# Kernel tuning notes

Hardware: AMD Instinct MI355X
Metric: run time of the kernel (lower is better)

## Reference

```python
import jax, jax.numpy as jnp
import numpy as np

PC_MIN = jnp.array([-51.2, -51.2, -5.0], dtype=jnp.float32)
PC_MAX = jnp.array([51.2, 51.2, 3.0], dtype=jnp.float32)
H0, W0 = 900, 1600  # original image size used for grid normalization
EPS = 1e-5


def grid_sample_2d(feats, gx, gy):
    # feats: (N,C,H,W); gx,gy: (N,Q) normalized [-1,1]; bilinear, align_corners=False, zero padding
    N, C, H, W = feats.shape
    x = ((gx + 1.0) * W - 1.0) / 2.0
    y = ((gy + 1.0) * H - 1.0) / 2.0
    x0 = jnp.floor(x)
    y0 = jnp.floor(y)
    ff = feats.reshape(N, C, H * W)
    out = jnp.zeros((N, C, gx.shape[1]), dtype=feats.dtype)
    for dx in (0, 1):
        for dy in (0, 1):
            xi = x0 + dx
            yi = y0 + dy
            w = (1.0 - jnp.abs(x - xi)) * (1.0 - jnp.abs(y - yi))
            inb = (xi >= 0) & (xi < W) & (yi >= 0) & (yi < H)
            idx = (jnp.clip(yi, 0, H - 1) * W + jnp.clip(xi, 0, W - 1)).astype(jnp.int32)
            g = jnp.take_along_axis(ff, idx[:, None, :], axis=2)  # (N,C,Q)
            out = out + g * (w * inb)[:, None, :]
    return out


def grid_sample_3d(feats, gx, gy, gz):
    # feats: (B,C,Z,Y,X); gx->X, gy->Y, gz->Z; trilinear, align_corners=False, zero padding
    B, C, Z, Y, X = feats.shape
    x = ((gx + 1.0) * X - 1.0) / 2.0
    y = ((gy + 1.0) * Y - 1.0) / 2.0
    z = ((gz + 1.0) * Z - 1.0) / 2.0
    x0 = jnp.floor(x)
    y0 = jnp.floor(y)
    z0 = jnp.floor(z)
    ff = feats.reshape(B, C, Z * Y * X)
    out = jnp.zeros((B, C, gx.shape[1]), dtype=feats.dtype)
    for dx in (0, 1):
        for dy in (0, 1):
            for dz in (0, 1):
                xi = x0 + dx
                yi = y0 + dy
                zi = z0 + dz
                w = (1.0 - jnp.abs(x - xi)) * (1.0 - jnp.abs(y - yi)) * (1.0 - jnp.abs(z - zi))
                inb = (xi >= 0) & (xi < X) & (yi >= 0) & (yi < Y) & (zi >= 0) & (zi < Z)
                idx = ((jnp.clip(zi, 0, Z - 1) * Y + jnp.clip(yi, 0, Y - 1)) * X + jnp.clip(xi, 0, X - 1)).astype(jnp.int32)
                g = jnp.take_along_axis(ff, idx[:, None, :], axis=2)  # (B,C,Q)
                out = out + g * (w * inb)[:, None, :]
    return out


def layer_norm(x, g, b):
    mu = x.mean(-1, keepdims=True)
    var = ((x - mu) ** 2).mean(-1, keepdims=True)
    return (x - mu) * jax.lax.rsqrt(var + 1e-5) * g + b


def setup_inputs() -> dict:
    key = jax.random.key(0)
    ks = jax.random.split(key, 20)
    B, Q, C, N = 2, 900, 256, 6
    H, W = 112, 200
    Z, Y, X = 10, 128, 128
    s = 0.02
    return {
        'query': jax.random.normal(ks[0], (B, Q, C), jnp.float32),
        'reference_points': jax.random.uniform(ks[1], (B, Q, 3), jnp.float32),
        'img_feats': jax.random.normal(ks[2], (B, N, C, H, W), jnp.float32),
        'lidar_feats': jax.random.normal(ks[3], (B, C, Z, Y, X), jnp.float32),
        'lidar2img': jax.random.normal(ks[4], (B, N, 4, 4), jnp.float32),
        'cam_w': jax.random.normal(ks[5], (C, C), jnp.float32) * s,
        'cam_b': jnp.zeros((C,), jnp.float32),
        'lidar_w': jax.random.normal(ks[6], (C, C), jnp.float32) * s,
        'lidar_b': jnp.zeros((C,), jnp.float32),
        'att_w1': jax.random.normal(ks[7], (C, C // 4), jnp.float32) * s,
        'att_b1': jnp.zeros((C // 4,), jnp.float32),
        'att_w2': jax.random.normal(ks[8], (C // 4, 2), jnp.float32) * s,
        'att_b2': jnp.zeros((2,), jnp.float32),
        'fus_w1': jax.random.normal(ks[9], (2 * C, C), jnp.float32) * s,
        'fus_b1': jnp.zeros((C,), jnp.float32),
        'ln_g': jnp.ones((C,), jnp.float32),
        'ln_b': jnp.zeros((C,), jnp.float32),
        'fus_w2': jax.random.normal(ks[10], (C, C), jnp.float32) * s,
        'fus_b2': jnp.zeros((C,), jnp.float32),
    }


def reference(query, reference_points, img_feats, lidar_feats, lidar2img,
              cam_w, cam_b, lidar_w, lidar_b, att_w1, att_b1, att_w2, att_b2,
              fus_w1, fus_b1, ln_g, ln_b, fus_w2, fus_b2):
    B, Q, _ = query.shape
    N, C = img_feats.shape[1], img_feats.shape[2]
    # ---- camera branch: 3D -> 2D projection + bilinear sample + masked mean over cams ----
    abs_pts = reference_points * (PC_MAX - PC_MIN) + PC_MIN
    homo = jnp.concatenate([abs_pts, jnp.ones_like(abs_pts[..., :1])], -1)  # (B,Q,4)
    cam = jnp.einsum('bnij,bqj->bnqi', lidar2img, homo)  # (B,N,Q,4)
    depth = cam[..., 2]
    dmask = depth > EPS
    dclamp = jnp.maximum(depth, EPS)
    u_n = 2.0 * (cam[..., 0] / dclamp) / (W0 - 1) - 1.0
    v_n = 2.0 * (cam[..., 1] / dclamp) / (H0 - 1) - 1.0
    valid = (u_n >= -1) & (u_n <= 1) & (v_n >= -1) & (v_n <= 1) & dmask  # (B,N,Q)
    Hf, Wf = img_feats.shape[-2], img_feats.shape[-1]
    samp = grid_sample_2d(img_feats.reshape(B * N, C, Hf, Wf),
                          u_n.reshape(B * N, Q), v_n.reshape(B * N, Q))  # (B*N,C,Q)
    samp = samp.reshape(B, N, C, Q).transpose(0, 3, 1, 2)  # (B,Q,N,C)
    vm = valid.transpose(0, 2, 1)[..., None].astype(samp.dtype)  # (B,Q,N,1)
    feat_cam = (samp * vm).sum(2) / jnp.maximum(vm.sum(2), 1.0)  # (B,Q,C)
    # ---- LiDAR branch: 3D trilinear sample ----
    g = reference_points * 2.0 - 1.0
    feat_lid = grid_sample_3d(lidar_feats, g[..., 0], g[..., 1], g[..., 2]).transpose(0, 2, 1)  # (B,Q,C)
    # ---- projections + adaptive gated fusion ----
    feat_cam = feat_cam @ cam_w + cam_b
    feat_lid = feat_lid @ lidar_w + lidar_b
    h = jax.nn.relu(query @ att_w1 + att_b1)
    w = jax.nn.softmax(h @ att_w2 + att_b2, axis=-1)  # (B,Q,2)
    fused = jnp.concatenate([w[..., 0:1] * feat_cam, w[..., 1:2] * feat_lid], -1)
    h2 = jax.nn.relu(layer_norm(fused @ fus_w1 + fus_b1, ln_g, ln_b))  # dropout is identity in eval
    return h2 @ fus_w2 + fus_b2
```

## Files before the change

kernel.cpp:

```cpp
#include <hip/hip_runtime.h>

#define QN 900
#define CN 256
#define NCAM 6
#define HF 112
#define WF 200
#define ZL 10
#define YL 128
#define XL 128
#define R 2

__global__ __launch_bounds__(256) void mafs_fused(
    const float* __restrict__ query,
    const float* __restrict__ rp,
    const float* __restrict__ imgf,
    const float* __restrict__ lidf,
    const float* __restrict__ l2i,
    const float* __restrict__ cam_w, const float* __restrict__ cam_b,
    const float* __restrict__ lid_w, const float* __restrict__ lid_b,
    const float* __restrict__ att_w1, const float* __restrict__ att_b1,
    const float* __restrict__ att_w2, const float* __restrict__ att_b2,
    const float* __restrict__ fus_w1, const float* __restrict__ fus_b1,
    const float* __restrict__ ln_g, const float* __restrict__ ln_b,
    const float* __restrict__ fus_w2, const float* __restrict__ fus_b2,
    float* __restrict__ out)
{
  const int blk = blockIdx.x;
  const int q0  = blk * R;
  const int b   = q0 / QN;
  const int tid = threadIdx.x;
  const int lane = tid & 63, wv = tid >> 6;

  __shared__ float s_q[R*CN];
  __shared__ float s_a[CN*R], s_b[CN*R], s_t[CN*R];
  __shared__ float s_hp[4*64];
  __shared__ float s_w0[R], s_w1[R];
  __shared__ float s_red[16];

  #pragma unroll
  for (int r = 0; r < R; ++r)
    s_q[r*CN + tid] = query[(size_t)(q0+r)*CN + tid];
  __syncthreads();

  {
    const int r  = wv & 1;
    const int kh = wv >> 1;
    const float* qrow = s_q + r*CN + kh*128;
    const float* w1p  = att_w1 + (size_t)kh*128*64;
    float h = 0.f;
    #pragma unroll 4
    for (int k = 0; k < 128; ++k) h += qrow[k] * w1p[k*64 + lane];
    s_hp[wv*64 + lane] = h;
  }
  __syncthreads();
  if (wv < R) {
    const int r = wv;
    float h = s_hp[r*64 + lane] + s_hp[(r+2)*64 + lane] + att_b1[lane];
    h = fmaxf(h, 0.f);
    float l0 = h * att_w2[2*lane], l1 = h * att_w2[2*lane+1];
    #pragma unroll
    for (int o = 32; o > 0; o >>= 1) { l0 += __shfl_down(l0,o); l1 += __shfl_down(l1,o); }
    if (lane == 0) {
      l0 += att_b2[0]; l1 += att_b2[1];
      const float m  = fmaxf(l0, l1);
      const float e0 = expf(l0 - m), e1 = expf(l1 - m);
      const float inv = 1.f / (e0 + e1);
      s_w0[r] = e0 * inv; s_w1[r] = e1 * inv;
    }
  }

  float rxx[R], ryy[R], rzz[R];
  #pragma unroll
  for (int r = 0; r < R; ++r) {
    rxx[r] = rp[(q0+r)*3+0];
    ryy[r] = rp[(q0+r)*3+1];
    rzz[r] = rp[(q0+r)*3+2];
  }

  float lv[R][8], lw[R][8];
  {
    const float* lbase = lidf + ((size_t)(b*CN) + tid) * (ZL*YL*XL);
    #pragma unroll
    for (int r = 0; r < R; ++r) {
      const float x = rxx[r]*(float)XL - 0.5f;
      const float y = ryy[r]*(float)YL - 0.5f;
      const float z = rzz[r]*(float)ZL - 0.5f;
      const float x0f = floorf(x), y0f = floorf(y), z0f = floorf(z);
      const int x0=(int)x0f, y0=(int)y0f, z0=(int)z0f;
      const float fx=x-x0f, fy=y-y0f, fz=z-z0f;
      const float wx[2]={1.f-fx,fx}, wy[2]={1.f-fy,fy}, wz[2]={1.f-fz,fz};
      #pragma unroll
      for (int dz = 0; dz < 2; ++dz)
        #pragma unroll
        for (int dy = 0; dy < 2; ++dy)
          #pragma unroll
          for (int dx = 0; dx < 2; ++dx) {
            const int xi=x0+dx, yi=y0+dy, zi=z0+dz;
            const bool ib = (xi>=0)&&(xi<XL)&&(yi>=0)&&(yi<YL)&&(zi>=0)&&(zi<ZL);
            const int xc=min(max(xi,0),XL-1);
            const int yc=min(max(yi,0),YL-1);
            const int zc=min(max(zi,0),ZL-1);
            const int i=(dz*2+dy)*2+dx;
            lv[r][i] = lbase[(zc*YL+yc)*XL+xc];
            lw[r][i] = ib ? wx[dx]*wy[dy]*wz[dz] : 0.f;
          }
    }
  }

  float fc[R] = {0.f,0.f}, cnt[R] = {0.f,0.f};
  #pragma unroll
  for (int n = 0; n < NCAM; ++n) {
    const float* M = l2i + (size_t)(b*NCAM + n)*16;
    const float m0=M[0],m1=M[1],m2=M[2],m3=M[3];
    const float m4=M[4],m5=M[5],m6=M[6],m7=M[7];
    const float m8=M[8],m9=M[9],m10=M[10],m11=M[11];
    #pragma unroll
    for (int r = 0; r < R; ++r) {
      const float ax = rxx[r]*102.4f - 51.2f;
      const float ay = ryy[r]*102.4f - 51.2f;
      const float az = rzz[r]*8.0f   - 5.0f;
      const float c0 = m0*ax + m1*ay + m2 *az + m3;
      const float c1 = m4*ax + m5*ay + m6 *az + m7;
      const float c2 = m8*ax + m9*ay + m10*az + m11;
      const float dc = fmaxf(c2, 1e-5f);
      const float u = 2.0f * (c0 / dc) / 1599.0f - 1.0f;
      const float v = 2.0f * (c1 / dc) /  899.0f - 1.0f;
      const bool valid = (u >= -1.f) && (u <= 1.f) && (v >= -1.f) && (v <= 1.f)
                         && (c2 > 1e-5f);
      if (valid) {
        cnt[r] += 1.f;
        const float x = ((u + 1.f)*(float)WF - 1.f)*0.5f;
        const float y = ((v + 1.f)*(float)HF - 1.f)*0.5f;
        const float x0f = floorf(x), y0f = floorf(y);
        const int x0=(int)x0f, y0=(int)y0f;
        const float fx=x-x0f, fy=y-y0f;
        const bool xb0=(x0>=0)&&(x0<WF), xb1=(x0+1<WF)&&(x0+1>=0);
        const bool yb0=(y0>=0)&&(y0<HF), yb1=(y0+1<HF)&&(y0+1>=0);
        const float w00 = (xb0&&yb0) ? (1.f-fx)*(1.f-fy) : 0.f;
        const float w10 = (xb1&&yb0) ? fx*(1.f-fy)       : 0.f;
        const float w01 = (xb0&&yb1) ? (1.f-fx)*fy       : 0.f;
        const float w11 = (xb1&&yb1) ? fx*fy             : 0.f;
        const int xc0=min(max(x0,0),WF-1),  xc1=min(max(x0+1,0),WF-1);
        const int yc0=min(max(y0,0),HF-1),  yc1=min(max(y0+1,0),HF-1);
        const float* fb = imgf + ((size_t)((b*NCAM + n)*CN) + tid)*(HF*WF);
        const float t00 = fb[yc0*WF + xc0];
        const float t10 = fb[yc0*WF + xc1];
        const float t01 = fb[yc1*WF + xc0];
        const float t11 = fb[yc1*WF + xc1];
        fc[r] += w00*t00 + w10*t10 + w01*t01 + w11*t11;
      }
    }
  }
  #pragma unroll
  for (int r = 0; r < R; ++r) fc[r] /= fmaxf(cnt[r], 1.f);

  float fl[R];
  #pragma unroll
  for (int r = 0; r < R; ++r) {
    float s = 0.f;
    #pragma unroll
    for (int i = 0; i < 8; ++i) s += lw[r][i] * lv[r][i];
    fl[r] = s;
  }

  #pragma unroll
  for (int r = 0; r < R; ++r) { s_a[tid*R + r] = fc[r]; s_b[tid*R + r] = fl[r]; }
  __syncthreads();

  float pc[R] = {0,0}, pl[R] = {0,0};
  #pragma unroll 4
  for (int k = 0; k < CN; ++k) {
    const float wc = cam_w[k*CN + tid];
    const float wl = lid_w[k*CN + tid];
    const float2 xa = *(const float2*)&s_a[k*R];
    const float2 xb = *(const float2*)&s_b[k*R];
    pc[0] += xa.x*wc; pc[1] += xa.y*wc;
    pl[0] += xb.x*wl; pl[1] += xb.y*wl;
  }
  const float pcb = cam_b[tid], plb = lid_b[tid];
  __syncthreads();
  #pragma unroll
  for (int r = 0; r < R; ++r) {
    s_a[tid*R + r] = s_w0[r] * (pc[r] + pcb);
    s_b[tid*R + r] = s_w1[r] * (pl[r] + plb);
  }
  __syncthreads();

  float t1[R] = {0,0};
  #pragma unroll 2
  for (int k = 0; k < CN; ++k) {
    const float wA = fus_w1[k*CN + tid];
    const float wB = fus_w1[(size_t)(CN + k)*CN + tid];
    const float2 xa = *(const float2*)&s_a[k*R];
    const float2 xb = *(const float2*)&s_b[k*R];
    t1[0] += xa.x*wA + xb.x*wB;
    t1[1] += xa.y*wA + xb.y*wB;
  }
  {
    const float bb = fus_b1[tid];
    t1[0] += bb; t1[1] += bb;
  }

  #pragma unroll
  for (int r = 0; r < R; ++r) {
    float s1 = t1[r];
    #pragma unroll
    for (int o = 32; o > 0; o >>= 1) s1 += __shfl_down(s1, o);
    if (lane == 0) s_red[r*4 + wv] = s1;
  }
  __syncthreads();
  float mu[R];
  #pragma unroll
  for (int r = 0; r < R; ++r)
    mu[r] = (s_red[r*4+0]+s_red[r*4+1]+s_red[r*4+2]+s_red[r*4+3]) * (1.f/256.f);
  #pragma unroll
  for (int r = 0; r < R; ++r) {
    const float d = t1[r] - mu[r];
    float s2 = d*d;
    #pragma unroll
    for (int o = 32; o > 0; o >>= 1) s2 += __shfl_down(s2, o);
    if (lane == 0) s_red[8 + r*4 + wv] = s2;
  }
  __syncthreads();
  {
    const float g = ln_g[tid], be = ln_b[tid];
    #pragma unroll
    for (int r = 0; r < R; ++r) {
      const float var = (s_red[8+r*4+0]+s_red[8+r*4+1]+s_red[8+r*4+2]+s_red[8+r*4+3]) * (1.f/256.f);
      const float ri = rsqrtf(var + 1e-5f);
      s_t[tid*R + r] = fmaxf((t1[r] - mu[r]) * ri * g + be, 0.f);
    }
  }
  __syncthreads();

  float o[R] = {0,0};
  #pragma unroll 4
  for (int k = 0; k < CN; ++k) {
    const float w = fus_w2[k*CN + tid];
    const float2 xt = *(const float2*)&s_t[k*R];
    o[0] += xt.x*w; o[1] += xt.y*w;
  }
  const float ob = fus_b2[tid];
  #pragma unroll
  for (int r = 0; r < R; ++r)
    out[(size_t)(q0+r)*CN + tid] = o[r] + ob;
}

extern "C" void kernel_launch(void* const* d_in, const int* in_sizes, int n_in,
                              void* d_out, int out_size, void* d_ws, size_t ws_size,
                              hipStream_t stream) {
  const float* query   = (const float*)d_in[0];
  const float* rpts    = (const float*)d_in[1];
  const float* imgf    = (const float*)d_in[2];
  const float* lidf    = (const float*)d_in[3];
  const float* l2i     = (const float*)d_in[4];
  const float* cam_w   = (const float*)d_in[5];
  const float* cam_b   = (const float*)d_in[6];
  const float* lid_w   = (const float*)d_in[7];
  const float* lid_b   = (const float*)d_in[8];
  const float* att_w1  = (const float*)d_in[9];
  const float* att_b1  = (const float*)d_in[10];
  const float* att_w2  = (const float*)d_in[11];
  const float* att_b2  = (const float*)d_in[12];
  const float* fus_w1  = (const float*)d_in[13];
  const float* fus_b1  = (const float*)d_in[14];
  const float* ln_g    = (const float*)d_in[15];
  const float* ln_b    = (const float*)d_in[16];
  const float* fus_w2  = (const float*)d_in[17];
  const float* fus_b2  = (const float*)d_in[18];
  float* out = (float*)d_out;

  dim3 grid((2*QN)/R);
  dim3 block(256);
  mafs_fused<<<grid, block, 0, stream>>>(
      query, rpts, imgf, lidf, l2i,
      cam_w, cam_b, lid_w, lid_b,
      att_w1, att_b1, att_w2, att_b2,
      fus_w1, fus_b1, ln_g, ln_b, fus_w2, fus_b2, out);
}
```

Measured before the change: 119.0 us.

## Process four queries per block with 512 threads split into two halves

```diff
diff --git a/kernel.cpp b/kernel.cpp
--- a/kernel.cpp
+++ b/kernel.cpp
@@ -8,9 +8,10 @@
 #define ZL 10
 #define YL 128
 #define XL 128
-#define R 2
-
-__global__ __launch_bounds__(256) void mafs_fused(
+#define R 4
+#define NT 512
+
+__global__ __launch_bounds__(NT, 4) void mafs_fused(
     const float* __restrict__ query,
     const float* __restrict__ rp,
     const float* __restrict__ imgf,
@@ -29,35 +30,36 @@
   const int q0  = blk * R;
   const int b   = q0 / QN;
   const int tid = threadIdx.x;
-  const int lane = tid & 63, wv = tid >> 6;
+  const int c    = tid & 255;
+  const int h    = tid >> 8;
+  const int lane = tid & 63;
+  const int w    = tid >> 6;
 
   __shared__ float s_q[R*CN];
   __shared__ float s_a[CN*R], s_b[CN*R], s_t[CN*R];
-  __shared__ float s_hp[4*64];
+  __shared__ float s_hp[8*64];
   __shared__ float s_w0[R], s_w1[R];
-  __shared__ float s_red[16];
-
-  #pragma unroll
-  for (int r = 0; r < R; ++r)
-    s_q[r*CN + tid] = query[(size_t)(q0+r)*CN + tid];
-  __syncthreads();
-
-  {
-    const int r  = wv & 1;
-    const int kh = wv >> 1;
-    const float* qrow = s_q + r*CN + kh*128;
-    const float* w1p  = att_w1 + (size_t)kh*128*64;
-    float h = 0.f;
+  __shared__ float s_red[2*R*4];
+
+  #pragma unroll
+  for (int i = 0; i < 2; ++i)
+    s_q[i*NT + tid] = query[(size_t)q0*CN + i*NT + tid];
+  __syncthreads();
+
+  {
+    const int rw = w & 3, kh = w >> 2;
+    const float* qrow = s_q + rw*CN + kh*128;
+    const float* w1p  = att_w1 + (size_t)(kh*128)*64;
+    float hh = 0.f;
     #pragma unroll 4
-    for (int k = 0; k < 128; ++k) h += qrow[k] * w1p[k*64 + lane];
-    s_hp[wv*64 + lane] = h;
-  }
-  __syncthreads();
-  if (wv < R) {
-    const int r = wv;
-    float h = s_hp[r*64 + lane] + s_hp[(r+2)*64 + lane] + att_b1[lane];
-    h = fmaxf(h, 0.f);
-    float l0 = h * att_w2[2*lane], l1 = h * att_w2[2*lane+1];
+    for (int k = 0; k < 128; ++k) hh += qrow[k] * w1p[k*64 + lane];
+    s_hp[w*64 + lane] = hh;
+  }
+  __syncthreads();
+  if (w < R) {
+    float hh = s_hp[w*64 + lane] + s_hp[(w+4)*64 + lane] + att_b1[lane];
+    hh = fmaxf(hh, 0.f);
+    float l0 = hh * att_w2[2*lane], l1 = hh * att_w2[2*lane+1];
     #pragma unroll
     for (int o = 32; o > 0; o >>= 1) { l0 += __shfl_down(l0,o); l1 += __shfl_down(l1,o); }
     if (lane == 0) {
@@ -65,26 +67,27 @@
       const float m  = fmaxf(l0, l1);
       const float e0 = expf(l0 - m), e1 = expf(l1 - m);
       const float inv = 1.f / (e0 + e1);
-      s_w0[r] = e0 * inv; s_w1[r] = e1 * inv;
-    }
-  }
-
-  float rxx[R], ryy[R], rzz[R];
-  #pragma unroll
-  for (int r = 0; r < R; ++r) {
-    rxx[r] = rp[(q0+r)*3+0];
-    ryy[r] = rp[(q0+r)*3+1];
-    rzz[r] = rp[(q0+r)*3+2];
-  }
-
-  float lv[R][8], lw[R][8];
-  {
-    const float* lbase = lidf + ((size_t)(b*CN) + tid) * (ZL*YL*XL);
-    #pragma unroll
-    for (int r = 0; r < R; ++r) {
-      const float x = rxx[r]*(float)XL - 0.5f;
-      const float y = ryy[r]*(float)YL - 0.5f;
-      const float z = rzz[r]*(float)ZL - 0.5f;
+      s_w0[w] = e0 * inv; s_w1[w] = e1 * inv;
+    }
+  }
+
+  float rxx[2], ryy[2], rzz[2];
+  #pragma unroll
+  for (int i = 0; i < 2; ++i) {
+    const int r = 2*h + i;
+    rxx[i] = rp[(q0+r)*3+0];
+    ryy[i] = rp[(q0+r)*3+1];
+    rzz[i] = rp[(q0+r)*3+2];
+  }
+
+  float lv[2][8], lw_[2][8];
+  {
+    const float* lbase = lidf + ((size_t)(b*CN) + c) * (ZL*YL*XL);
+    #pragma unroll
+    for (int i = 0; i < 2; ++i) {
+      const float x = rxx[i]*(float)XL - 0.5f;
+      const float y = ryy[i]*(float)YL - 0.5f;
+      const float z = rzz[i]*(float)ZL - 0.5f;
       const float x0f = floorf(x), y0f = floorf(y), z0f = floorf(z);
       const int x0=(int)x0f, y0=(int)y0f, z0=(int)z0f;
       const float fx=x-x0f, fy=y-y0f, fz=z-z0f;
@@ -100,14 +103,14 @@
             const int xc=min(max(xi,0),XL-1);
             const int yc=min(max(yi,0),YL-1);
             const int zc=min(max(zi,0),ZL-1);
-            const int i=(dz*2+dy)*2+dx;
-            lv[r][i] = lbase[(zc*YL+yc)*XL+xc];
-            lw[r][i] = ib ? wx[dx]*wy[dy]*wz[dz] : 0.f;
+            const int t=(dz*2+dy)*2+dx;
+            lv[i][t]  = lbase[(zc*YL+yc)*XL+xc];
+            lw_[i][t] = ib ? wx[dx]*wy[dy]*wz[dz] : 0.f;
           }
     }
   }
 
-  float fc[R] = {0.f,0.f}, cnt[R] = {0.f,0.f};
+  float fc[2] = {0.f,0.f}, cnt[2] = {0.f,0.f};
   #pragma unroll
   for (int n = 0; n < NCAM; ++n) {
     const float* M = l2i + (size_t)(b*NCAM + n)*16;
@@ -115,10 +118,10 @@
     const float m4=M[4],m5=M[5],m6=M[6],m7=M[7];
     const float m8=M[8],m9=M[9],m10=M[10],m11=M[11];
     #pragma unroll
-    for (int r = 0; r < R; ++r) {
-      const float ax = rxx[r]*102.4f - 51.2f;
-      const float ay = ryy[r]*102.4f - 51.2f;
-      const float az = rzz[r]*8.0f   - 5.0f;
+    for (int i = 0; i < 2; ++i) {
+      const float ax = rxx[i]*102.4f - 51.2f;
+      const float ay = ryy[i]*102.4f - 51.2f;
+      const float az = rzz[i]*8.0f   - 5.0f;
       const float c0 = m0*ax + m1*ay + m2 *az + m3;
       const float c1 = m4*ax + m5*ay + m6 *az + m7;
       const float c2 = m8*ax + m9*ay + m10*az + m11;
@@ -128,7 +131,7 @@
       const bool valid = (u >= -1.f) && (u <= 1.f) && (v >= -1.f) && (v <= 1.f)
                          && (c2 > 1e-5f);
       if (valid) {
-        cnt[r] += 1.f;
+        cnt[i] += 1.f;
         const float x = ((u + 1.f)*(float)WF - 1.f)*0.5f;
         const float y = ((v + 1.f)*(float)HF - 1.f)*0.5f;
         const float x0f = floorf(x), y0f = floorf(y);
@@ -142,108 +145,115 @@
         const float w11 = (xb1&&yb1) ? fx*fy             : 0.f;
         const int xc0=min(max(x0,0),WF-1),  xc1=min(max(x0+1,0),WF-1);
         const int yc0=min(max(y0,0),HF-1),  yc1=min(max(y0+1,0),HF-1);
-        const float* fb = imgf + ((size_t)((b*NCAM + n)*CN) + tid)*(HF*WF);
+        const float* fb = imgf + ((size_t)((b*NCAM + n)*CN) + c)*(HF*WF);
         const float t00 = fb[yc0*WF + xc0];
         const float t10 = fb[yc0*WF + xc1];
         const float t01 = fb[yc1*WF + xc0];
         const float t11 = fb[yc1*WF + xc1];
-        fc[r] += w00*t00 + w10*t10 + w01*t01 + w11*t11;
+        fc[i] += w00*t00 + w10*t10 + w01*t01 + w11*t11;
       }
     }
   }
   #pragma unroll
-  for (int r = 0; r < R; ++r) fc[r] /= fmaxf(cnt[r], 1.f);
-
-  float fl[R];
-  #pragma unroll
-  for (int r = 0; r < R; ++r) {
+  for (int i = 0; i < 2; ++i) fc[i] /= fmaxf(cnt[i], 1.f);
+
+  float fl[2];
+  #pragma unroll
+  for (int i = 0; i < 2; ++i) {
     float s = 0.f;
     #pragma unroll
-    for (int i = 0; i < 8; ++i) s += lw[r][i] * lv[r][i];
-    fl[r] = s;
-  }
-
-  #pragma unroll
-  for (int r = 0; r < R; ++r) { s_a[tid*R + r] = fc[r]; s_b[tid*R + r] = fl[r]; }
-  __syncthreads();
-
-  float pc[R] = {0,0}, pl[R] = {0,0};
+    for (int t = 0; t < 8; ++t) s += lw_[i][t] * lv[i][t];
+    fl[i] = s;
+  }
+
+  #pragma unroll
+  for (int i = 0; i < 2; ++i) {
+    s_a[c*R + 2*h + i] = fc[i];
+    s_b[c*R + 2*h + i] = fl[i];
+  }
+  __syncthreads();
+
+  float pc[2] = {0,0}, pl[2] = {0,0};
+  #pragma unroll 8
+  for (int k = 0; k < CN; ++k) {
+    const float wc = cam_w[k*CN + c];
+    const float wl = lid_w[k*CN + c];
+    const float2 xa = *(const float2*)&s_a[k*R + 2*h];
+    const float2 xb = *(const float2*)&s_b[k*R + 2*h];
+    pc[0] += xa.x*wc; pc[1] += xa.y*wc;
+    pl[0] += xb.x*wl; pl[1] += xb.y*wl;
+  }
+  const float pcb = cam_b[c], plb = lid_b[c];
+  __syncthreads();
+  #pragma unroll
+  for (int i = 0; i < 2; ++i) {
+    const int r = 2*h + i;
+    s_a[c*R + r] = s_w0[r] * (pc[i] + pcb);
+    s_b[c*R + r] = s_w1[r] * (pl[i] + plb);
+  }
+  __syncthreads();
+
+  float t1[2] = {0,0};
   #pragma unroll 4
   for (int k = 0; k < CN; ++k) {
-    const float wc = cam_w[k*CN + tid];
-    const float wl = lid_w[k*CN + tid];
-    const float2 xa = *(const float2*)&s_a[k*R];
-    const float2 xb = *(const float2*)&s_b[k*R];
-    pc[0] += xa.x*wc; pc[1] += xa.y*wc;
-    pl[0] += xb.x*wl; pl[1] += xb.y*wl;
-  }
-  const float pcb = cam_b[tid], plb = lid_b[tid];
-  __syncthreads();
-  #pragma unroll
-  for (int r = 0; r < R; ++r) {
-    s_a[tid*R + r] = s_w0[r] * (pc[r] + pcb);
-    s_b[tid*R + r] = s_w1[r] * (pl[r] + plb);
-  }
-  __syncthreads();
-
-  float t1[R] = {0,0};
-  #pragma unroll 2
-  for (int k = 0; k < CN; ++k) {
-    const float wA = fus_w1[k*CN + tid];
-    const float wB = fus_w1[(size_t)(CN + k)*CN + tid];
-    const float2 xa = *(const float2*)&s_a[k*R];
-    const float2 xb = *(const float2*)&s_b[k*R];
+    const float wA = fus_w1[k*CN + c];
+    const float wB = fus_w1[(size_t)(CN + k)*CN + c];
+    const float2 xa = *(const float2*)&s_a[k*R + 2*h];
+    const float2 xb = *(const float2*)&s_b[k*R + 2*h];
     t1[0] += xa.x*wA + xb.x*wB;
     t1[1] += xa.y*wA + xb.y*wB;
   }
   {
-    const float bb = fus_b1[tid];
+    const float bb = fus_b1[c];
     t1[0] += bb; t1[1] += bb;
   }
 
   #pragma unroll
-  for (int r = 0; r < R; ++r) {
-    float s1 = t1[r];
+  for (int i = 0; i < 2; ++i) {
+    float s1 = t1[i];
     #pragma unroll
     for (int o = 32; o > 0; o >>= 1) s1 += __shfl_down(s1, o);
-    if (lane == 0) s_red[r*4 + wv] = s1;
-  }
-  __syncthreads();
-  float mu[R];
-  #pragma unroll
-  for (int r = 0; r < R; ++r)
-    mu[r] = (s_red[r*4+0]+s_red[r*4+1]+s_red[r*4+2]+s_red[r*4+3]) * (1.f/256.f);
-  #pragma unroll
-  for (int r = 0; r < R; ++r) {
-    const float d = t1[r] - mu[r];
+    if (lane == 0) s_red[(2*h+i)*4 + (w & 3)] = s1;
+  }
+  __syncthreads();
+  float mu[2];
+  #pragma unroll
+  for (int i = 0; i < 2; ++i) {
+    const int r = 2*h + i;
+    mu[i] = (s_red[r*4+0]+s_red[r*4+1]+s_red[r*4+2]+s_red[r*4+3]) * (1.f/256.f);
+  }
+  #pragma unroll
+  for (int i = 0; i < 2; ++i) {
+    const float d = t1[i] - mu[i];
     float s2 = d*d;
     #pragma unroll
     for (int o = 32; o > 0; o >>= 1) s2 += __shfl_down(s2, o);
-    if (lane == 0) s_red[8 + r*4 + wv] = s2;
-  }
-  __syncthreads();
-  {
-    const float g = ln_g[tid], be = ln_b[tid];
-    #pragma unroll
-    for (int r = 0; r < R; ++r) {
-      const float var = (s_red[8+r*4+0]+s_red[8+r*4+1]+s_red[8+r*4+2]+s_red[8+r*4+3]) * (1.f/256.f);
+    if (lane == 0) s_red[16 + (2*h+i)*4 + (w & 3)] = s2;
+  }
+  __syncthreads();
+  {
+    const float g = ln_g[c], be = ln_b[c];
+    #pragma unroll
+    for (int i = 0; i < 2; ++i) {
+      const int r = 2*h + i;
+      const float var = (s_red[16+r*4+0]+s_red[16+r*4+1]+s_red[16+r*4+2]+s_red[16+r*4+3]) * (1.f/256.f);
       const float ri = rsqrtf(var + 1e-5f);
-      s_t[tid*R + r] = fmaxf((t1[r] - mu[r]) * ri * g + be, 0.f);
-    }
-  }
-  __syncthreads();
-
-  float o[R] = {0,0};
+      s_t[c*R + r] = fmaxf((t1[i] - mu[i]) * ri * g + be, 0.f);
+    }
+  }
+  __syncthreads();
+
+  float o[2] = {0,0};
   #pragma unroll 4
   for (int k = 0; k < CN; ++k) {
-    const float w = fus_w2[k*CN + tid];
-    const float2 xt = *(const float2*)&s_t[k*R];
-    o[0] += xt.x*w; o[1] += xt.y*w;
-  }
-  const float ob = fus_b2[tid];
-  #pragma unroll
-  for (int r = 0; r < R; ++r)
-    out[(size_t)(q0+r)*CN + tid] = o[r] + ob;
+    const float wgt = fus_w2[k*CN + c];
+    const float2 xt = *(const float2*)&s_t[k*R + 2*h];
+    o[0] += xt.x*wgt; o[1] += xt.y*wgt;
+  }
+  const float ob = fus_b2[c];
+  #pragma unroll
+  for (int i = 0; i < 2; ++i)
+    out[(size_t)(q0 + 2*h + i)*CN + c] = o[i] + ob;
 }
 
 extern "C" void kernel_launch(void* const* d_in, const int* in_sizes, int n_in,
@@ -271,7 +281,7 @@
   float* out = (float*)d_out;
 
   dim3 grid((2*QN)/R);
-  dim3 block(256);
+  dim3 block(NT);
   mafs_fused<<<grid, block, 0, stream>>>(
       query, rpts, imgf, lidf, l2i,
       cam_w, cam_b, lid_w, lid_b,
```

Measured after the change: 96.20 us (median of 2 runs). -19.2%, faster.
